# Performance work log

Hardware: AMD Instinct MI355X
Metric: run time of the kernel (lower is better)

Reference implementation:

```python
import jax, jax.numpy as jnp
import numpy as np

EPS = 1e-6
H = 12  # num_heads


def _rms(x, w):
    return x / jnp.sqrt(jnp.mean(x * x, axis=-1, keepdims=True) + EPS) * w


def _rot_half(x):
    x1, x2 = jnp.split(x, 2, axis=-1)
    return jnp.concatenate([-x2, x1], axis=-1)


def _rope(t, cos, sin):
    # t: [B,H,N,hd]; cos/sin: [N,hd] broadcast
    return t * cos + _rot_half(t) * sin


def setup_inputs() -> dict:
    key = jax.random.key(0)
    B, N, D, Nc = 1, 2048, 768, 16
    hd = D // H
    mh = 4 * D
    ks = jax.random.split(key, 16)
    s = 0.02
    g = lambda k, shape, sc=1.0: jax.random.normal(k, shape, dtype=jnp.float32) * sc
    # real RoPE tables (half-duplicated layout to match rotate_half)
    inv = 1.0 / (10000.0 ** (np.arange(hd // 2, dtype=np.float64) / (hd // 2)))
    ang = np.arange(N, dtype=np.float64)[:, None] * inv[None, :]
    cos = jnp.asarray(np.concatenate([np.cos(ang), np.cos(ang)], -1), dtype=jnp.float32)
    sin = jnp.asarray(np.concatenate([np.sin(ang), np.sin(ang)], -1), dtype=jnp.float32)
    return {
        'x': g(ks[0], (B, N, D)),
        'c': g(ks[1], (B, D)),
        'cond': g(ks[2], (B, Nc, D)),
        'rope_cos': cos,
        'rope_sin': sin,
        'norm1_w': jnp.ones((D,), jnp.float32),
        'norm2_w': jnp.ones((D,), jnp.float32),
        'norm3_w': jnp.ones((D,), jnp.float32),
        'cond_norm_w': jnp.ones((D,), jnp.float32),
        'sa_qkv_w': g(ks[3], (3 * D, D), s),
        'sa_proj_w': g(ks[4], (D, D), s),
        'sa_proj_b': jnp.zeros((D,), jnp.float32),
        'sa_qn_w': jnp.ones((hd,), jnp.float32),
        'sa_kn_w': jnp.ones((hd,), jnp.float32),
        'ca_q_w': g(ks[5], (D, D), s),
        'ca_k_w': g(ks[6], (D, D), s),
        'ca_v_w': g(ks[7], (D, D), s),
        'ca_proj_w': g(ks[8], (D, D), s),
        'ca_proj_b': jnp.zeros((D,), jnp.float32),
        'ca_qn_w': jnp.ones((hd,), jnp.float32),
        'ca_kn_w': jnp.ones((hd,), jnp.float32),
        'mlp_w1': g(ks[9], (mh, D), s),
        'mlp_w2': g(ks[10], (D, mh), s),
        'mlp_w3': g(ks[11], (mh, D), s),
        'ada_w': g(ks[12], (9 * D, D), s),
        'ada_b': jnp.zeros((9 * D,), jnp.float32),
    }


def reference(x, c, cond, rope_cos, rope_sin, norm1_w, norm2_w, norm3_w, cond_norm_w,
              sa_qkv_w, sa_proj_w, sa_proj_b, sa_qn_w, sa_kn_w,
              ca_q_w, ca_k_w, ca_v_w, ca_proj_w, ca_proj_b, ca_qn_w, ca_kn_w,
              mlp_w1, mlp_w2, mlp_w3, ada_w, ada_b):
    B, N, D = x.shape
    hd = D // H
    scale = hd ** -0.5

    # adaLN modulation: SiLU(c) -> Linear -> 9 chunks of [B, D]
    mod = jax.nn.silu(c) @ ada_w.T + ada_b
    (sh_msa, sc_msa, g_msa, sh_ca, sc_ca, g_ca,
     sh_mlp, sc_mlp, g_mlp) = jnp.split(mod, 9, axis=1)

    def modulate(h, sh, sc):
        return h * (1.0 + sc[:, None, :]) + sh[:, None, :]

    # ---- self-attention with QK-norm + RoPE ----
    h = modulate(_rms(x, norm1_w), sh_msa, sc_msa)
    qkv = (h @ sa_qkv_w.T).reshape(B, N, 3, H, hd).transpose(2, 0, 3, 1, 4)  # [3,B,H,N,hd]
    q, k, v = qkv[0], qkv[1], qkv[2]
    q = _rope(_rms(q, sa_qn_w), rope_cos, rope_sin)
    k = _rope(_rms(k, sa_kn_w), rope_cos, rope_sin)
    attn = jax.nn.softmax(jnp.einsum('bhid,bhjd->bhij', q, k) * scale, axis=-1)
    o = jnp.einsum('bhij,bhjd->bhid', attn, v).transpose(0, 2, 1, 3).reshape(B, N, D)
    x = x + g_msa[:, None, :] * (o @ sa_proj_w.T + sa_proj_b)

    # ---- cross-attention (RoPE on q only) ----
    h = modulate(_rms(x, norm2_w), sh_ca, sc_ca)
    cn = _rms(cond, cond_norm_w)
    Nc = cond.shape[1]
    q = (h @ ca_q_w.T).reshape(B, N, H, hd).transpose(0, 2, 1, 3)
    k = (cn @ ca_k_w.T).reshape(B, Nc, H, hd).transpose(0, 2, 1, 3)
    v = (cn @ ca_v_w.T).reshape(B, Nc, H, hd).transpose(0, 2, 1, 3)
    q = _rope(_rms(q, ca_qn_w), rope_cos, rope_sin)
    k = _rms(k, ca_kn_w)
    attn = jax.nn.softmax(jnp.einsum('bhid,bhjd->bhij', q, k) * scale, axis=-1)
    o = jnp.einsum('bhij,bhjd->bhid', attn, v).transpose(0, 2, 1, 3).reshape(B, N, D)
    x = x + g_ca[:, None, :] * (o @ ca_proj_w.T + ca_proj_b)

    # ---- SwiGLU MLP ----
    h = modulate(_rms(x, norm3_w), sh_mlp, sc_mlp)
    x = x + g_mlp[:, None, :] * ((jax.nn.silu(h @ mlp_w1.T) * (h @ mlp_w3.T)) @ mlp_w2.T)
    return x
```

## Files before the change

### kernel.cpp

```cpp
#include <hip/hip_runtime.h>

typedef unsigned short u16;
typedef unsigned int u32;
typedef __attribute__((ext_vector_type(8))) short s16x8;
typedef __attribute__((ext_vector_type(4))) float f32x4;
typedef __attribute__((ext_vector_type(4))) int i32x4;

#define PS 1572864

#define OFF_SAQKV  0
#define OFF_SAPROJ 1769472
#define OFF_CAQ    2359296
#define OFF_CAPROJ 2949120
#define OFF_W1     3538944
#define OFF_W2     5898240
#define OFF_W3     8257536

static __device__ __forceinline__ float bf2f(u16 u) {
    return __uint_as_float(((u32)u) << 16);
}
static __device__ __forceinline__ u16 f2bf(float f) {
    u32 x = __float_as_uint(f);
    return (u16)((x + 0x7fffu + ((x >> 16) & 1u)) >> 16);
}
static __device__ __forceinline__ i32x4 pack8(float4 a, float4 b) {
    u32 p0 = (u32)f2bf(a.x) | ((u32)f2bf(a.y) << 16);
    u32 p1 = (u32)f2bf(a.z) | ((u32)f2bf(a.w) << 16);
    u32 p2 = (u32)f2bf(b.x) | ((u32)f2bf(b.y) << 16);
    u32 p3 = (u32)f2bf(b.z) | ((u32)f2bf(b.w) << 16);
    return (i32x4){(int)p0, (int)p1, (int)p2, (int)p3};
}
static __device__ __forceinline__ float wave_sum(float v) {
#pragma unroll
    for (int off = 32; off > 0; off >>= 1) v += __shfl_xor(v, off);
    return v;
}
static __device__ __forceinline__ void gload16(const void* g, void* l) {
    __builtin_amdgcn_global_load_lds((const __attribute__((address_space(1))) void*)g,
                                     (__attribute__((address_space(3))) void*)l, 16, 0, 0);
}

__global__ __launch_bounds__(256) void cvt_ada(const float* __restrict__ s0,
                                               const float* __restrict__ s1,
                                               const float* __restrict__ s2,
                                               const float* __restrict__ s3,
                                               const float* __restrict__ s4,
                                               const float* __restrict__ s5,
                                               const float* __restrict__ s6,
                                               u16* __restrict__ wall,
                                               const float* __restrict__ c,
                                               const float* __restrict__ adaw,
                                               const float* __restrict__ adab,
                                               float* __restrict__ mod) {
    const int bid = blockIdx.x;
    const int tid = threadIdx.x;
    if (bid < 5184) {
        int u = bid * 256 + tid;
        const float* src;
        int rel;
        if (u < 221184)       { src = s0; rel = u; }
        else if (u < 294912)  { src = s1; rel = u - 221184; }
        else if (u < 368640)  { src = s2; rel = u - 294912; }
        else if (u < 442368)  { src = s3; rel = u - 368640; }
        else if (u < 737280)  { src = s4; rel = u - 442368; }
        else if (u < 1032192) { src = s5; rel = u - 737280; }
        else                  { src = s6; rel = u - 1032192; }
        float4 a = *(const float4*)(src + (size_t)rel * 8);
        float4 b = *(const float4*)(src + (size_t)rel * 8 + 4);
        *(i32x4*)(wall + (size_t)u * 8) = pack8(a, b);
    } else {
        int wid = (bid - 5184) * 4 + (tid >> 6);
        int lane = tid & 63;
        float sum = 0.f;
#pragma unroll
        for (int i = 0; i < 12; ++i) {
            float cv = c[i * 64 + lane];
            cv = cv / (1.f + __expf(-cv));
            sum += cv * adaw[(size_t)wid * 768 + i * 64 + lane];
        }
        sum = wave_sum(sum);
        if (lane == 0) mod[wid] = sum + adab[wid];
    }
}

__global__ __launch_bounds__(256) void rms_mod(const float* __restrict__ x,
                                               const float* __restrict__ w,
                                               const float* __restrict__ mod, int chunk,
                                               u16* __restrict__ out) {
    const int row = blockIdx.x;
    const int tid = threadIdx.x;
    const float* xr = x + (size_t)row * 768;
    float v0 = xr[tid], v1 = xr[256 + tid], v2 = xr[512 + tid];
    float ss = wave_sum(v0 * v0 + v1 * v1 + v2 * v2);
    __shared__ float red[4];
    if ((tid & 63) == 0) red[tid >> 6] = ss;
    __syncthreads();
    float rn = rsqrtf((red[0] + red[1] + red[2] + red[3]) * (1.f / 768.f) + 1e-6f);
    const float* sh = mod + chunk * 768;
    const float* sc = sh + 768;
    u16* orow = out + (size_t)row * 768;
    orow[tid]       = f2bf(v0 * rn * w[tid]       * (1.f + sc[tid])       + sh[tid]);
    orow[256 + tid] = f2bf(v1 * rn * w[256 + tid] * (1.f + sc[256 + tid]) + sh[256 + tid]);
    orow[512 + tid] = f2bf(v2 * rn * w[512 + tid] * (1.f + sc[512 + tid]) + sh[512 + tid]);
}

template <int EPI, int BN>
__global__ __launch_bounds__(256) void gemm_bt4(const u16* __restrict__ A,
                                                const u16* __restrict__ Wb,
                                                int M, int N, int K,
                                                float* outf, u16* outb,
                                                const float* resid,
                                                const float* __restrict__ gate,
                                                const float* __restrict__ bias,
                                                int C, int R, int nxc) {
    constexpr int NB = BN / 32;
    __shared__ __align__(16) u16 As[2][128 * 32];
    __shared__ __align__(16) u16 Bs[2][BN * 32];
    const int tid = threadIdx.x;
    const int lane = tid & 63;
    const int w = tid >> 6;
    const int wr = w >> 1, wc = w & 1;
    const int sub = blockIdx.x;
    const int xcd = sub & 7, idx = sub >> 3;
    const int cx = xcd % nxc, cy = xcd / nxc;
    const int col0 = (cx * C + idx % C) * BN;
    const int row0 = (cy * R + idx / C) << 7;

    const int r0u = tid >> 2, s0u = (tid & 3) ^ (r0u & 3);
    const int r1u = (tid + 256) >> 2, s1u = (tid & 3) ^ (r1u & 3);
    const u16* a0 = A + (size_t)(row0 + r0u) * K + s0u * 8;
    const u16* a1 = A + (size_t)(row0 + r1u) * K + s1u * 8;
    const u16* b0 = Wb + (size_t)(col0 + r0u) * K + s0u * 8;
    const u16* b1 = Wb + (size_t)(col0 + r1u) * K + s1u * 8;

    f32x4 acc[4][NB];
#pragma unroll
    for (int m = 0; m < 4; ++m)
#pragma unroll
        for (int n = 0; n < NB; ++n) acc[m][n] = (f32x4){0.f, 0.f, 0.f, 0.f};

    const int nt = K >> 5;
    int cur = 0;
#define G4_STAGE(buf, k0)                                   \
    {                                                       \
        char* ad = (char*)As[buf] + w * 1024;               \
        char* bd = (char*)Bs[buf] + w * 1024;               \
        gload16(a0 + (k0), ad);                             \
        gload16(a1 + (k0), ad + 4096);                      \
        gload16(b0 + (k0), bd);                             \
        if constexpr (BN == 128) gload16(b1 + (k0), bd + 4096); \
    }
    G4_STAGE(0, 0)
    for (int t = 0; t < nt; ++t) {
        __syncthreads();
        if (t + 1 < nt) G4_STAGE(cur ^ 1, (t + 1) << 5)
        s16x8 af[4], bfv[NB];
#pragma unroll
        for (int m = 0; m < 4; ++m) {
            int ra = wr * 64 + m * 16 + (lane & 15);
            int u = (lane >> 4) ^ (ra & 3);
            af[m] = *(const s16x8*)((const char*)As[cur] + ra * 64 + u * 16);
        }
#pragma unroll
        for (int n = 0; n < NB; ++n) {
            int cb = wc * (BN / 2) + n * 16 + (lane & 15);
            int u = (lane >> 4) ^ (cb & 3);
            bfv[n] = *(const s16x8*)((const char*)Bs[cur] + cb * 64 + u * 16);
        }
#pragma unroll
        for (int m = 0; m < 4; ++m)
#pragma unroll
            for (int n = 0; n < NB; ++n)
                acc[m][n] = __builtin_amdgcn_mfma_f32_16x16x32_bf16(af[m], bfv[n], acc[m][n], 0, 0, 0);
        cur ^= 1;
    }
#undef G4_STAGE
#pragma unroll
    for (int m = 0; m < 4; ++m) {
#pragma unroll
        for (int n = 0; n < NB; ++n) {
#pragma unroll
            for (int i = 0; i < 4; ++i) {
                int r = row0 + wr * 64 + m * 16 + (lane >> 4) * 4 + i;
                int cc = col0 + wc * (BN / 2) + n * 16 + (lane & 15);
                size_t idx2 = (size_t)r * N + cc;
                float v = acc[m][n][i];
                if constexpr (EPI == 0) {
                    outf[idx2] = v;
                } else if constexpr (EPI == 1) {
                    outb[idx2] = f2bf(v);
                } else if constexpr (EPI == 2) {
                    float b = bias ? bias[cc] : 0.f;
                    outf[idx2] = resid[idx2] + gate[cc] * (v + b);
                }
            }
        }
    }
}

__global__ __launch_bounds__(256) void gemm_sk4(const u16* __restrict__ A,
                                                const u16* __restrict__ Wb,
                                                int M, int N, int K,
                                                u16* __restrict__ pz,
                                                int C, int R, int nxc,
                                                int nsub, int kslice) {
    __shared__ __align__(16) u16 As[2][128 * 32];
    __shared__ __align__(16) u16 Bs[2][64 * 32];
    const int tid = threadIdx.x;
    const int lane = tid & 63;
    const int w = tid >> 6;
    const int wr = w >> 1, wc = w & 1;
    const int sub = blockIdx.x % nsub;
    const int z = blockIdx.x / nsub;
    const int xcd = sub & 7, idx = sub >> 3;
    const int cx = xcd % nxc, cy = xcd / nxc;
    const int col0 = (cx * C + idx % C) << 6;
    const int row0 = (cy * R + idx / C) << 7;
    const int kbase = z * kslice;

    const int r0u = tid >> 2, s0u = (tid & 3) ^ (r0u & 3);
    const int r1u = (tid + 256) >> 2, s1u = (tid & 3) ^ (r1u & 3);
    const u16* a0 = A + (size_t)(row0 + r0u) * K + kbase + s0u * 8;
    const u16* a1 = A + (size_t)(row0 + r1u) * K + kbase + s1u * 8;
    const u16* b0 = Wb + (size_t)(col0 + r0u) * K + kbase + s0u * 8;

    f32x4 acc[4][2];
#pragma unroll
    for (int m = 0; m < 4; ++m)
#pragma unroll
        for (int n = 0; n < 2; ++n) acc[m][n] = (f32x4){0.f, 0.f, 0.f, 0.f};

    const int nt = kslice >> 5;
    int cur = 0;
#define SK_STAGE(buf, k0)                                   \
    {                                                       \
        char* ad = (char*)As[buf] + w * 1024;               \
        char* bd = (char*)Bs[buf] + w * 1024;               \
        gload16(a0 + (k0), ad);                             \
        gload16(a1 + (k0), ad + 4096);                      \
        gload16(b0 + (k0), bd);                             \
    }
    SK_STAGE(0, 0)
    for (int t = 0; t < nt; ++t) {
        __syncthreads();
        if (t + 1 < nt) SK_STAGE(cur ^ 1, (t + 1) << 5)
        s16x8 af[4], bfv[2];
#pragma unroll
        for (int m = 0; m < 4; ++m) {
            int ra = wr * 64 + m * 16 + (lane & 15);
            int u = (lane >> 4) ^ (ra & 3);
            af[m] = *(const s16x8*)((const char*)As[cur] + ra * 64 + u * 16);
        }
#pragma unroll
        for (int n = 0; n < 2; ++n) {
            int cb = wc * 32 + n * 16 + (lane & 15);
            int u = (lane >> 4) ^ (cb & 3);
            bfv[n] = *(const s16x8*)((const char*)Bs[cur] + cb * 64 + u * 16);
        }
#pragma unroll
        for (int m = 0; m < 4; ++m)
#pragma unroll
            for (int n = 0; n < 2; ++n)
                acc[m][n] = __builtin_amdgcn_mfma_f32_16x16x32_bf16(af[m], bfv[n], acc[m][n], 0, 0, 0);
        cur ^= 1;
    }
#undef SK_STAGE
    u16* po = pz + (size_t)z * PS;
#pragma unroll
    for (int m = 0; m < 4; ++m)
#pragma unroll
        for (int n = 0; n < 2; ++n)
#pragma unroll
            for (int i = 0; i < 4; ++i) {
                int r = row0 + wr * 64 + m * 16 + (lane >> 4) * 4 + i;
                int cc = col0 + wc * 32 + n * 16 + (lane & 15);
                po[(size_t)r * N + cc] = f2bf(acc[m][n][i]);
            }
}

template <int MODE>
__global__ __launch_bounds__(256) void comb4(const u16* __restrict__ pz,
                                             const float* __restrict__ resid,
                                             const float* __restrict__ gate,
                                             const float* __restrict__ bias,
                                             float* __restrict__ outf) {
    int base = (blockIdx.x * 256 + threadIdx.x) * 8;
    int col = base % 768;
    s16x8 p0 = *(const s16x8*)(pz + base);
    s16x8 p1 = *(const s16x8*)(pz + PS + base);
    s16x8 p2 = *(const s16x8*)(pz + 2 * PS + base);
    s16x8 p3 = *(const s16x8*)(pz + 3 * PS + base);
    float o[8];
#pragma unroll
    for (int e = 0; e < 8; ++e) {
        float s = (bf2f((u16)p0[e]) + bf2f((u16)p1[e])) +
                  (bf2f((u16)p2[e]) + bf2f((u16)p3[e]));
        if constexpr (MODE == 0) {
            o[e] = s;
        } else {
            float bb = bias ? bias[col + e] : 0.f;
            o[e] = resid[base + e] + gate[col + e] * (s + bb);
        }
    }
    *(float4*)(outf + base) = (float4){o[0], o[1], o[2], o[3]};
    *(float4*)(outf + base + 4) = (float4){o[4], o[5], o[6], o[7]};
}

__global__ __launch_bounds__(256) void comb_rms(const u16* __restrict__ pz,
                                                const float* __restrict__ resid,
                                                const float* __restrict__ gate,
                                                const float* __restrict__ bias,
                                                const float* __restrict__ mod, int chunk,
                                                const float* __restrict__ w,
                                                float* __restrict__ outf,
                                                u16* __restrict__ outb) {
    const int row = blockIdx.x;
    const int tid = threadIdx.x;
    float val[3];
    float ss = 0.f;
#pragma unroll
    for (int j = 0; j < 3; ++j) {
        int col = tid + j * 256;
        size_t ix = (size_t)row * 768 + col;
        float s = (bf2f(pz[ix]) + bf2f(pz[PS + ix])) +
                  (bf2f(pz[2 * PS + ix]) + bf2f(pz[3 * PS + ix]));
        float bb = bias ? bias[col] : 0.f;
        float v = resid[ix] + gate[col] * (s + bb);
        val[j] = v;
        ss += v * v;
        outf[ix] = v;
    }
    ss = wave_sum(ss);
    __shared__ float red[4];
    if ((tid & 63) == 0) red[tid >> 6] = ss;
    __syncthreads();
    float rn = rsqrtf((red[0] + red[1] + red[2] + red[3]) * (1.f / 768.f) + 1e-6f);
    const float* sh = mod + chunk * 768;
    const float* sc = sh + 768;
#pragma unroll
    for (int j = 0; j < 3; ++j) {
        int col = tid + j * 256;
        size_t ix = (size_t)row * 768 + col;
        outb[ix] = f2bf(val[j] * rn * w[col] * (1.f + sc[col]) + sh[col]);
    }
}

__global__ __launch_bounds__(256) void comb_qrope(const u16* __restrict__ pz,
                                                  const float* __restrict__ qnw,
                                                  const float* __restrict__ cosT,
                                                  const float* __restrict__ sinT,
                                                  float* __restrict__ qb) {
    int wid = blockIdx.x * 4 + (threadIdx.x >> 6);
    int lane = threadIdx.x & 63;
    int n = wid / 12, h = wid % 12;
    size_t ix = (size_t)n * 768 + h * 64 + lane;
    float v = (bf2f(pz[ix]) + bf2f(pz[PS + ix])) +
              (bf2f(pz[2 * PS + ix]) + bf2f(pz[3 * PS + ix]));
    float ss = wave_sum(v * v);
    float vn = v * rsqrtf(ss * (1.f / 64.f) + 1e-6f) * qnw[lane];
    float part = __shfl_xor(vn, 32);
    float rot = (lane < 32) ? -part : part;
    qb[ix] = vn * cosT[n * 64 + lane] + rot * sinT[n * 64 + lane];
}

__global__ __launch_bounds__(256) void gemm_w13(const u16* __restrict__ A,
                                                const u16* __restrict__ W1,
                                                const u16* __restrict__ W3,
                                                int M, int N, int K,
                                                u16* __restrict__ outb,
                                                int C, int R, int nxc) {
    __shared__ __align__(16) u16 As[2][128 * 32];
    __shared__ __align__(16) u16 B1s[2][64 * 32];
    __shared__ __align__(16) u16 B3s[2][64 * 32];
    const int tid = threadIdx.x;
    const int lane = tid & 63;
    const int w = tid >> 6;
    const int wr = w >> 1, wc = w & 1;
    const int sub = blockIdx.x;
    const int xcd = sub & 7, idx = sub >> 3;
    const int cx = xcd % nxc, cy = xcd / nxc;
    const int col0 = (cx * C + idx % C) << 6;
    const int row0 = (cy * R + idx / C) << 7;

    const int r0u = tid >> 2, s0u = (tid & 3) ^ (r0u & 3);
    const int r1u = (tid + 256) >> 2, s1u = (tid & 3) ^ (r1u & 3);
    const u16* a0 = A + (size_t)(row0 + r0u) * K + s0u * 8;
    const u16* a1 = A + (size_t)(row0 + r1u) * K + s1u * 8;
    const u16* b1p = W1 + (size_t)(col0 + r0u) * K + s0u * 8;
    const u16* b3p = W3 + (size_t)(col0 + r0u) * K + s0u * 8;

    f32x4 acc1[4][2], acc3[4][2];
#pragma unroll
    for (int m = 0; m < 4; ++m)
#pragma unroll
        for (int n = 0; n < 2; ++n) {
            acc1[m][n] = (f32x4){0.f, 0.f, 0.f, 0.f};
            acc3[m][n] = (f32x4){0.f, 0.f, 0.f, 0.f};
        }

    const int nt = K >> 5;
    int cur = 0;
#define W13_STAGE(buf, k0)                                  \
    {                                                       \
        char* ad = (char*)As[buf] + w * 1024;               \
        char* bd1 = (char*)B1s[buf] + w * 1024;             \
        char* bd3 = (char*)B3s[buf] + w * 1024;             \
        gload16(a0 + (k0), ad);                             \
        gload16(a1 + (k0), ad + 4096);                      \
        gload16(b1p + (k0), bd1);                           \
        gload16(b3p + (k0), bd3);                           \
    }
    W13_STAGE(0, 0)
    for (int t = 0; t < nt; ++t) {
        __syncthreads();
        if (t + 1 < nt) W13_STAGE(cur ^ 1, (t + 1) << 5)
        s16x8 af[4], b1v[2], b3v[2];
#pragma unroll
        for (int m = 0; m < 4; ++m) {
            int ra = wr * 64 + m * 16 + (lane & 15);
            int u = (lane >> 4) ^ (ra & 3);
            af[m] = *(const s16x8*)((const char*)As[cur] + ra * 64 + u * 16);
        }
#pragma unroll
        for (int n = 0; n < 2; ++n) {
            int cb = wc * 32 + n * 16 + (lane & 15);
            int u = (lane >> 4) ^ (cb & 3);
            b1v[n] = *(const s16x8*)((const char*)B1s[cur] + cb * 64 + u * 16);
            b3v[n] = *(const s16x8*)((const char*)B3s[cur] + cb * 64 + u * 16);
        }
#pragma unroll
        for (int m = 0; m < 4; ++m)
#pragma unroll
            for (int n = 0; n < 2; ++n) {
                acc1[m][n] = __builtin_amdgcn_mfma_f32_16x16x32_bf16(af[m], b1v[n], acc1[m][n], 0, 0, 0);
                acc3[m][n] = __builtin_amdgcn_mfma_f32_16x16x32_bf16(af[m], b3v[n], acc3[m][n], 0, 0, 0);
            }
        cur ^= 1;
    }
#undef W13_STAGE
#pragma unroll
    for (int m = 0; m < 4; ++m)
#pragma unroll
        for (int n = 0; n < 2; ++n)
#pragma unroll
            for (int i = 0; i < 4; ++i) {
                int r = row0 + wr * 64 + m * 16 + (lane >> 4) * 4 + i;
                int cc = col0 + wc * 32 + n * 16 + (lane & 15);
                float v1 = acc1[m][n][i];
                float g = v1 / (1.f + __expf(-v1));
                outb[(size_t)r * N + cc] = f2bf(g * acc3[m][n][i]);
            }
}

__global__ __launch_bounds__(256) void qk_prep(u16* __restrict__ qkv,
                                               u16* __restrict__ vT,
                                               const float* __restrict__ qnw,
                                               const float* __restrict__ knw,
                                               const float* __restrict__ cosT,
                                               const float* __restrict__ sinT) {
    const int bid = blockIdx.x;
    const int tid = threadIdx.x;
    if (bid < 12288) {
        int wid = bid * 4 + (tid >> 6);
        int lane = tid & 63;
        int n = wid / 24;
        int rem = wid % 24;
        int which = rem / 12;
        int h = rem % 12;
        u16* p = qkv + (size_t)n * 2304 + which * 768 + h * 64 + lane;
        float v = bf2f(*p);
        float ss = wave_sum(v * v);
        const float* wv = which ? knw : qnw;
        float vn = v * rsqrtf(ss * (1.f / 64.f) + 1e-6f) * wv[lane];
        float part = __shfl_xor(vn, 32);
        float rot = (lane < 32) ? -part : part;
        *p = f2bf(vn * cosT[n * 64 + lane] + rot * sinT[n * 64 + lane]);
    } else {
        const int b2 = bid - 12288;
        const int kt = b2 & 31, h = b2 >> 5;
        __shared__ __align__(16) u16 tt[64][72];
        {
            int key = tid >> 2, qq = tid & 3;
            const u16* src = qkv + (size_t)(kt * 64 + key) * 2304 + 1536 + h * 64 + qq * 16;
            *(i32x4*)&tt[key][qq * 16]     = *(const i32x4*)src;
            *(i32x4*)&tt[key][qq * 16 + 8] = *(const i32x4*)(src + 8);
        }
        __syncthreads();
        {
            int d = tid >> 2, kq = tid & 3;
            s16x8 o0, o1;
#pragma unroll
            for (int e = 0; e < 8; ++e) o0[e] = (short)tt[kq * 16 + e][d];
#pragma unroll
            for (int e = 0; e < 8; ++e) o1[e] = (short)tt[kq * 16 + 8 + e][d];
            u16* dst = vT + (size_t)h * 131072 + (size_t)d * 2048 + kt * 64 + kq * 16;
            *(s16x8*)dst = o0;
            *(s16x8*)(dst + 8) = o1;
        }
    }
}

__global__ __launch_bounds__(256) void sa_attn_mfma(const u16* __restrict__ qkv,
                                                    const u16* __restrict__ vT,
                                                    u16* __restrict__ at,
                                                    float* __restrict__ pl) {
    const int h = blockIdx.y;
    const int r0 = blockIdx.x * 64;
    const int z = blockIdx.z;
    const int tid = threadIdx.x;
    const int lane = tid & 63;
    const int w = tid >> 6;
    __shared__ __align__(16) u16 Ks[2][64 * 64];
    __shared__ __align__(16) u16 Vs[2][64 * 64];
    __shared__ __align__(16) u16 Ps[4][16 * 64];

    s16x8 qf[2];
    {
        const u16* qrow = qkv + (size_t)(r0 + w * 16 + (lane & 15)) * 2304 + h * 64 + ((lane >> 4) * 8);
        qf[0] = *(const s16x8*)qrow;
        qf[1] = *(const s16x8*)(qrow + 32);
    }
    f32x4 oacc[4];
#pragma unroll
    for (int n = 0; n < 4; ++n) oacc[n] = (f32x4){0.f, 0.f, 0.f, 0.f};
    float lp[4] = {0.f, 0.f, 0.f, 0.f};

    const u16* ksrc[2];
    const u16* vsrc[2];
#pragma unroll
    for (int j = 0; j < 2; ++j) {
        int u = (w * 2 + j) * 64 + lane;
        int row = u >> 3, seg = (u & 7) ^ (row & 7);
        ksrc[j] = qkv + (size_t)(z * 512 + row) * 2304 + 768 + h * 64 + seg * 8;
        vsrc[j] = vT + (size_t)h * 131072 + (size_t)row * 2048 + z * 512 + seg * 8;
    }

#define SA_STAGE(buf, t_)                                          \
    {                                                              \
        char* kd = (char*)Ks[buf] + w * 2048;                      \
        char* vd = (char*)Vs[buf] + w * 2048;                      \
        gload16(ksrc[0] + (size_t)(t_) * 147456, kd);              \
        gload16(ksrc[1] + (size_t)(t_) * 147456, kd + 1024);       \
        gload16(vsrc[0] + (t_) * 64, vd);                          \
        gload16(vsrc[1] + (t_) * 64, vd + 1024);                   \
    }

    SA_STAGE(0, 0)
    int cur = 0;
    for (int t = 0; t < 8; ++t) {
        __syncthreads();
        if (t + 1 < 8) SA_STAGE(cur ^ 1, t + 1)

        f32x4 sacc[4];
#pragma unroll
        for (int n = 0; n < 4; ++n) sacc[n] = (f32x4){0.f, 0.f, 0.f, 0.f};
#pragma unroll
        for (int kk = 0; kk < 2; ++kk) {
#pragma unroll
            for (int n = 0; n < 4; ++n) {
                int key = n * 16 + (lane & 15);
                int d = kk * 32 + (lane >> 4) * 8;
                int boff = key * 128 + ((d * 2) ^ ((key & 7) << 4));
                s16x8 kf = *(const s16x8*)((const char*)Ks[cur] + boff);
                sacc[n] = __builtin_amdgcn_mfma_f32_16x16x32_bf16(qf[kk], kf, sacc[n], 0, 0, 0);
            }
        }
#pragma unroll
        for (int n = 0; n < 4; ++n) {
#pragma unroll
            for (int i = 0; i < 4; ++i) {
                float p = __expf(fmaf(sacc[n][i], 0.125f, -8.0f));
                lp[i] += p;
                int row = (lane >> 4) * 4 + i;
                int key = n * 16 + (lane & 15);
                int boff = row * 128 + ((key * 2) ^ ((row & 7) << 4));
                *(u16*)((char*)Ps[w] + boff) = f2bf(p);
            }
        }
#pragma unroll
        for (int kk = 0; kk < 2; ++kk) {
            int koff = kk * 32 + (lane >> 4) * 8;
            int prow = lane & 15;
            int pboff = prow * 128 + ((koff * 2) ^ ((prow & 7) << 4));
            s16x8 pf = *(const s16x8*)((const char*)Ps[w] + pboff);
#pragma unroll
            for (int n = 0; n < 4; ++n) {
                int d = n * 16 + (lane & 15);
                int vboff = d * 128 + ((koff * 2) ^ ((d & 7) << 4));
                s16x8 vf = *(const s16x8*)((const char*)Vs[cur] + vboff);
                oacc[n] = __builtin_amdgcn_mfma_f32_16x16x32_bf16(pf, vf, oacc[n], 0, 0, 0);
            }
        }
        cur ^= 1;
    }
#undef SA_STAGE
#pragma unroll
    for (int off = 1; off < 16; off <<= 1) {
#pragma unroll
        for (int i = 0; i < 4; ++i) lp[i] += __shfl_xor(lp[i], off);
    }
    u16* po = at + (size_t)z * PS;
#pragma unroll
    for (int n = 0; n < 4; ++n) {
#pragma unroll
        for (int i = 0; i < 4; ++i) {
            int r = r0 + w * 16 + (lane >> 4) * 4 + i;
            int d = n * 16 + (lane & 15);
            po[(size_t)r * 768 + h * 64 + d] = f2bf(oacc[n][i]);
        }
    }
    if ((lane & 15) == 0) {
#pragma unroll
        for (int i = 0; i < 4; ++i) {
            int r = r0 + w * 16 + (lane >> 4) * 4 + i;
            pl[z * 24576 + h * 2048 + r] = lp[i];
        }
    }
}

__global__ __launch_bounds__(256) void sa_combine4(const u16* __restrict__ at,
                                                   const float* __restrict__ pl,
                                                   u16* __restrict__ obuf) {
    int idx = blockIdx.x * 256 + threadIdx.x;
    int base = idx * 8;
    int row = base / 768;
    int col = base % 768;
    int h = col >> 6;
    float l = (pl[h * 2048 + row] + pl[24576 + h * 2048 + row]) +
              (pl[49152 + h * 2048 + row] + pl[73728 + h * 2048 + row]);
    float inv = 1.f / l;
    s16x8 a = *(const s16x8*)(at + base);
    s16x8 b = *(const s16x8*)(at + PS + base);
    s16x8 cc = *(const s16x8*)(at + 2 * PS + base);
    s16x8 d = *(const s16x8*)(at + 3 * PS + base);
    s16x8 o;
#pragma unroll
    for (int e = 0; e < 8; ++e) {
        float s = (bf2f((u16)a[e]) + bf2f((u16)b[e])) +
                  (bf2f((u16)cc[e]) + bf2f((u16)d[e]));
        o[e] = (short)f2bf(s * inv);
    }
    *(s16x8*)(obuf + base) = o;
}

__global__ __launch_bounds__(256) void ca_attn(const float* __restrict__ qb,
                                               const float* __restrict__ kca,
                                               const float* __restrict__ vca,
                                               u16* __restrict__ obuf) {
    int wid = blockIdx.x * 4 + (threadIdx.x >> 6);
    int lane = threadIdx.x & 63;
    int n = wid / 12, h = wid % 12;
    float qd = qb[(size_t)n * 768 + h * 64 + lane] * 0.125f;
    float s[16];
#pragma unroll
    for (int j = 0; j < 16; ++j) {
        float part = qd * kca[(size_t)j * 768 + h * 64 + lane];
        s[j] = wave_sum(part);
    }
    float mm = s[0];
#pragma unroll
    for (int j = 1; j < 16; ++j) mm = fmaxf(mm, s[j]);
    float l = 0.f;
#pragma unroll
    for (int j = 0; j < 16; ++j) { s[j] = __expf(s[j] - mm); l += s[j]; }
    float od = 0.f;
#pragma unroll
    for (int j = 0; j < 16; ++j) od += s[j] * vca[(size_t)j * 768 + h * 64 + lane];
    obuf[(size_t)n * 768 + h * 64 + lane] = f2bf(od / l);
}

__global__ __launch_bounds__(256) void cak_rms(float* __restrict__ kca,
                                               const float* __restrict__ knw) {
    int wid = blockIdx.x * 4 + (threadIdx.x >> 6);
    int lane = threadIdx.x & 63;
    int n = wid / 12, h = wid % 12;
    float* p = kca + (size_t)n * 768 + h * 64 + lane;
    float v = *p;
    float ss = wave_sum(v * v);
    *p = v * rsqrtf(ss * (1.f / 64.f) + 1e-6f) * knw[lane];
}

__global__ __launch_bounds__(256) void small_gemm_f(const float* __restrict__ cond,
                                                    const float* __restrict__ cnw,
                                                    const float* __restrict__ cakw,
                                                    const float* __restrict__ cavw,
                                                    float* __restrict__ kca,
                                                    float* __restrict__ vca) {
    int wid = blockIdx.x * 4 + (threadIdx.x >> 6);
    int lane = threadIdx.x & 63;
    int which = wid / 12288;
    int rem = wid % 12288;
    int rrow = rem / 768;
    int ocol = rem % 768;
    float cv[12];
    float ss = 0.f;
#pragma unroll
    for (int i = 0; i < 12; ++i) {
        cv[i] = cond[(size_t)rrow * 768 + i * 64 + lane];
        ss += cv[i] * cv[i];
    }
    ss = wave_sum(ss);
    float rn = rsqrtf(ss * (1.f / 768.f) + 1e-6f);
    const float* Wm = which ? cavw : cakw;
    float sum = 0.f;
#pragma unroll
    for (int i = 0; i < 12; ++i)
        sum += cv[i] * rn * cnw[i * 64 + lane] * Wm[(size_t)ocol * 768 + i * 64 + lane];
    sum = wave_sum(sum);
    if (lane == 0) (which ? vca : kca)[(size_t)rrow * 768 + ocol] = sum;
}

extern "C" void kernel_launch(void* const* d_in, const int* in_sizes, int n_in,
                              void* d_out, int out_size, void* d_ws, size_t ws_size,
                              hipStream_t stream) {
    const float* x     = (const float*)d_in[0];
    const float* c     = (const float*)d_in[1];
    const float* cond  = (const float*)d_in[2];
    const float* cosT  = (const float*)d_in[3];
    const float* sinT  = (const float*)d_in[4];
    const float* n1w   = (const float*)d_in[5];
    const float* n2w   = (const float*)d_in[6];
    const float* n3w   = (const float*)d_in[7];
    const float* cnw   = (const float*)d_in[8];
    const float* saqkvw  = (const float*)d_in[9];
    const float* saprojw = (const float*)d_in[10];
    const float* saprojb = (const float*)d_in[11];
    const float* saqnw   = (const float*)d_in[12];
    const float* saknw   = (const float*)d_in[13];
    const float* caqw    = (const float*)d_in[14];
    const float* cakw    = (const float*)d_in[15];
    const float* cavw    = (const float*)d_in[16];
    const float* caprojw = (const float*)d_in[17];
    const float* caprojb = (const float*)d_in[18];
    const float* caqnw   = (const float*)d_in[19];
    const float* caknw   = (const float*)d_in[20];
    const float* w1      = (const float*)d_in[21];
    const float* w2      = (const float*)d_in[22];
    const float* w3      = (const float*)d_in[23];
    const float* adaw    = (const float*)d_in[24];
    const float* adab    = (const float*)d_in[25];
    float* out = (float*)d_out;
    char* ws = (char*)d_ws;

    float* mod  = (float*)ws;
    u16* hbuf   = (u16*)(ws + 32768);
    u16* obuf   = (u16*)(ws + 3178496);
    char* R1    = ws + 6324224;
    u16* qkvb   = (u16*)R1;
    u16* vTb    = (u16*)(R1 + 9437184);
    float* qbuf = (float*)R1;
    u16* gbuf   = (u16*)R1;
    float* kca  = (float*)(ws + 18956288);
    float* vca  = (float*)(ws + 19005440);
    u16* WALL   = (u16*)(ws + 19054592);
    u16* AT     = (u16*)(ws + 40288256);
    float* PL4  = (float*)(ws + 52871168);
    u16* SKP    = (u16*)(ws + 53264384);

    cvt_ada<<<6912, 256, 0, stream>>>(saqkvw, saprojw, caqw, caprojw, w1, w2, w3,
                                      WALL, c, adaw, adab, mod);

    rms_mod<<<2048, 256, 0, stream>>>(x, n1w, mod, 0, hbuf);
    gemm_bt4<1, 64><<<576, 256, 0, stream>>>(hbuf, WALL + OFF_SAQKV, 2048, 2304, 768,
                                             nullptr, qkvb, nullptr, nullptr, nullptr,
                                             9, 8, 4);
    qk_prep<<<12672, 256, 0, stream>>>(qkvb, vTb, saqnw, saknw, cosT, sinT);
    sa_attn_mfma<<<dim3(32, 12, 4), 256, 0, stream>>>(qkvb, vTb, AT, PL4);
    sa_combine4<<<768, 256, 0, stream>>>(AT, PL4, obuf);
    gemm_sk4<<<768, 256, 0, stream>>>(obuf, WALL + OFF_SAPROJ, 2048, 768, 768,
                                      SKP, 6, 4, 2, 192, 192);
    comb_rms<<<2048, 256, 0, stream>>>(SKP, x, mod + 2 * 768, saprojb,
                                       mod, 3, n2w, out, hbuf);

    gemm_sk4<<<768, 256, 0, stream>>>(hbuf, WALL + OFF_CAQ, 2048, 768, 768,
                                      SKP, 6, 4, 2, 192, 192);
    comb_qrope<<<6144, 256, 0, stream>>>(SKP, caqnw, cosT, sinT, qbuf);
    small_gemm_f<<<6144, 256, 0, stream>>>(cond, cnw, cakw, cavw, kca, vca);
    cak_rms<<<48, 256, 0, stream>>>(kca, caknw);
    ca_attn<<<6144, 256, 0, stream>>>(qbuf, kca, vca, obuf);
    gemm_sk4<<<768, 256, 0, stream>>>(obuf, WALL + OFF_CAPROJ, 2048, 768, 768,
                                      SKP, 6, 4, 2, 192, 192);
    comb_rms<<<2048, 256, 0, stream>>>(SKP, out, mod + 5 * 768, caprojb,
                                       mod, 6, n3w, out, hbuf);

    gemm_w13<<<768, 256, 0, stream>>>(hbuf, WALL + OFF_W1, WALL + OFF_W3,
                                      2048, 3072, 768, gbuf, 12, 8, 4);
    gemm_sk4<<<768, 256, 0, stream>>>(gbuf, WALL + OFF_W2, 2048, 768, 3072,
                                      SKP, 6, 4, 2, 192, 768);
    comb4<2><<<768, 256, 0, stream>>>(SKP, out, mod + 8 * 768, nullptr, out);
}
```

Baseline: 222.3 us.

## Fuse QK norm, RoPE and V transpose into QKV GEMM epilogue; fold cond K/V into prologue

The QKV GEMM epilogue now stages each 128x64 tile in shared memory. There it applies per-head RMS norm and RoPE to the Q and K columns, and writes a transposed V copy directly, so the separate qk_prep kernel and its extra pass over qkv are gone. The cross-attention K/V projection of cond, together with its K RMS norm, moves into extra blocks of the initial conversion kernel, removing two launches. In exchange the GEMM epilogue carries more shared-memory traffic and a serial per-thread loop over 32 elements.

```diff
diff --git a/kernel.cpp b/kernel.cpp
--- a/kernel.cpp
+++ b/kernel.cpp
@@ -51,7 +51,14 @@
                                                const float* __restrict__ c,
                                                const float* __restrict__ adaw,
                                                const float* __restrict__ adab,
-                                               float* __restrict__ mod) {
+                                               float* __restrict__ mod,
+                                               const float* __restrict__ cond,
+                                               const float* __restrict__ cnw,
+                                               const float* __restrict__ cakw,
+                                               const float* __restrict__ cavw,
+                                               const float* __restrict__ caknw,
+                                               float* __restrict__ kca,
+                                               float* __restrict__ vca) {
     const int bid = blockIdx.x;
     const int tid = threadIdx.x;
     if (bid < 5184) {
@@ -68,7 +75,7 @@
         float4 a = *(const float4*)(src + (size_t)rel * 8);
         float4 b = *(const float4*)(src + (size_t)rel * 8 + 4);
         *(i32x4*)(wall + (size_t)u * 8) = pack8(a, b);
-    } else {
+    } else if (bid < 6912) {
         int wid = (bid - 5184) * 4 + (tid >> 6);
         int lane = tid & 63;
         float sum = 0.f;
@@ -80,6 +87,46 @@
         }
         sum = wave_sum(sum);
         if (lane == 0) mod[wid] = sum + adab[wid];
+    } else {
+        int b = bid - 6912;
+        int which = b / 192;
+        int rem = b % 192;
+        int rrow = rem / 12, h = rem % 12;
+        int w = tid >> 6, lane = tid & 63;
+        __shared__ float kvsh[64];
+        float cv[12];
+        float ss = 0.f;
+#pragma unroll
+        for (int i = 0; i < 12; ++i) {
+            cv[i] = cond[(size_t)rrow * 768 + i * 64 + lane];
+            ss += cv[i] * cv[i];
+        }
+        ss = wave_sum(ss);
+        float rn = rsqrtf(ss * (1.f / 768.f) + 1e-6f);
+#pragma unroll
+        for (int i = 0; i < 12; ++i) cv[i] = cv[i] * rn * cnw[i * 64 + lane];
+        const float* Wm = which ? cavw : cakw;
+#pragma unroll
+        for (int j = 0; j < 16; ++j) {
+            int ocol = h * 64 + w * 16 + j;
+            float d = 0.f;
+#pragma unroll
+            for (int i = 0; i < 12; ++i)
+                d += cv[i] * Wm[(size_t)ocol * 768 + i * 64 + lane];
+            d = wave_sum(d);
+            if (lane == 0) kvsh[w * 16 + j] = d;
+        }
+        __syncthreads();
+        if (tid < 64) {
+            float v = kvsh[lane];
+            if (which == 0) {
+                float sk = wave_sum(v * v);
+                v = v * rsqrtf(sk * (1.f / 64.f) + 1e-6f) * caknw[lane];
+                kca[(size_t)rrow * 768 + h * 64 + lane] = v;
+            } else {
+                vca[(size_t)rrow * 768 + h * 64 + lane] = v;
+            }
+        }
     }
 }
 
@@ -104,18 +151,19 @@
     orow[512 + tid] = f2bf(v2 * rn * w[512 + tid] * (1.f + sc[512 + tid]) + sh[512 + tid]);
 }
 
-template <int EPI, int BN>
-__global__ __launch_bounds__(256) void gemm_bt4(const u16* __restrict__ A,
+__global__ __launch_bounds__(256) void gemm_qkv(const u16* __restrict__ A,
                                                 const u16* __restrict__ Wb,
-                                                int M, int N, int K,
-                                                float* outf, u16* outb,
-                                                const float* resid,
-                                                const float* __restrict__ gate,
-                                                const float* __restrict__ bias,
+                                                u16* __restrict__ qkvb,
+                                                u16* __restrict__ vT,
+                                                const float* __restrict__ qnw,
+                                                const float* __restrict__ knw,
+                                                const float* __restrict__ cosT,
+                                                const float* __restrict__ sinT,
                                                 int C, int R, int nxc) {
-    constexpr int NB = BN / 32;
-    __shared__ __align__(16) u16 As[2][128 * 32];
-    __shared__ __align__(16) u16 Bs[2][BN * 32];
+    constexpr int K = 768, N = 2304;
+    __shared__ __align__(16) char smem[33792];
+    u16 (*As)[128 * 32] = (u16(*)[128 * 32])smem;
+    u16 (*Bs)[64 * 32] = (u16(*)[64 * 32])(smem + 16384);
     const int tid = threadIdx.x;
     const int lane = tid & 63;
     const int w = tid >> 6;
@@ -123,7 +171,7 @@
     const int sub = blockIdx.x;
     const int xcd = sub & 7, idx = sub >> 3;
     const int cx = xcd % nxc, cy = xcd / nxc;
-    const int col0 = (cx * C + idx % C) * BN;
+    const int col0 = (cx * C + idx % C) << 6;
     const int row0 = (cy * R + idx / C) << 7;
 
     const int r0u = tid >> 2, s0u = (tid & 3) ^ (r0u & 3);
@@ -131,30 +179,28 @@
     const u16* a0 = A + (size_t)(row0 + r0u) * K + s0u * 8;
     const u16* a1 = A + (size_t)(row0 + r1u) * K + s1u * 8;
     const u16* b0 = Wb + (size_t)(col0 + r0u) * K + s0u * 8;
-    const u16* b1 = Wb + (size_t)(col0 + r1u) * K + s1u * 8;
-
-    f32x4 acc[4][NB];
+
+    f32x4 acc[4][2];
 #pragma unroll
     for (int m = 0; m < 4; ++m)
 #pragma unroll
-        for (int n = 0; n < NB; ++n) acc[m][n] = (f32x4){0.f, 0.f, 0.f, 0.f};
+        for (int n = 0; n < 2; ++n) acc[m][n] = (f32x4){0.f, 0.f, 0.f, 0.f};
 
     const int nt = K >> 5;
     int cur = 0;
-#define G4_STAGE(buf, k0)                                   \
+#define QKV_STAGE(buf, k0)                                  \
     {                                                       \
         char* ad = (char*)As[buf] + w * 1024;               \
         char* bd = (char*)Bs[buf] + w * 1024;               \
         gload16(a0 + (k0), ad);                             \
         gload16(a1 + (k0), ad + 4096);                      \
         gload16(b0 + (k0), bd);                             \
-        if constexpr (BN == 128) gload16(b1 + (k0), bd + 4096); \
-    }
-    G4_STAGE(0, 0)
+    }
+    QKV_STAGE(0, 0)
     for (int t = 0; t < nt; ++t) {
         __syncthreads();
-        if (t + 1 < nt) G4_STAGE(cur ^ 1, (t + 1) << 5)
-        s16x8 af[4], bfv[NB];
+        if (t + 1 < nt) QKV_STAGE(cur ^ 1, (t + 1) << 5)
+        s16x8 af[4], bfv[2];
 #pragma unroll
         for (int m = 0; m < 4; ++m) {
             int ra = wr * 64 + m * 16 + (lane & 15);
@@ -162,38 +208,78 @@
             af[m] = *(const s16x8*)((const char*)As[cur] + ra * 64 + u * 16);
         }
 #pragma unroll
-        for (int n = 0; n < NB; ++n) {
-            int cb = wc * (BN / 2) + n * 16 + (lane & 15);
+        for (int n = 0; n < 2; ++n) {
+            int cb = wc * 32 + n * 16 + (lane & 15);
             int u = (lane >> 4) ^ (cb & 3);
             bfv[n] = *(const s16x8*)((const char*)Bs[cur] + cb * 64 + u * 16);
         }
 #pragma unroll
         for (int m = 0; m < 4; ++m)
 #pragma unroll
-            for (int n = 0; n < NB; ++n)
+            for (int n = 0; n < 2; ++n)
                 acc[m][n] = __builtin_amdgcn_mfma_f32_16x16x32_bf16(af[m], bfv[n], acc[m][n], 0, 0, 0);
         cur ^= 1;
     }
-#undef G4_STAGE
-#pragma unroll
-    for (int m = 0; m < 4; ++m) {
-#pragma unroll
-        for (int n = 0; n < NB; ++n) {
-#pragma unroll
-            for (int i = 0; i < 4; ++i) {
-                int r = row0 + wr * 64 + m * 16 + (lane >> 4) * 4 + i;
-                int cc = col0 + wc * (BN / 2) + n * 16 + (lane & 15);
-                size_t idx2 = (size_t)r * N + cc;
-                float v = acc[m][n][i];
-                if constexpr (EPI == 0) {
-                    outf[idx2] = v;
-                } else if constexpr (EPI == 1) {
-                    outb[idx2] = f2bf(v);
-                } else if constexpr (EPI == 2) {
-                    float b = bias ? bias[cc] : 0.f;
-                    outf[idx2] = resid[idx2] + gate[cc] * (v + b);
+#undef QKV_STAGE
+    __syncthreads();
+
+    const int region = col0 / 768;
+    const int h = (col0 % 768) >> 6;
+    if (region < 2) {
+        float (*T)[66] = (float(*)[66])smem;
+#pragma unroll
+        for (int m = 0; m < 4; ++m)
+#pragma unroll
+            for (int n = 0; n < 2; ++n)
+#pragma unroll
+                for (int i = 0; i < 4; ++i)
+                    T[wr * 64 + m * 16 + (lane >> 4) * 4 + i]
+                     [wc * 32 + n * 16 + (lane & 15)] = acc[m][n][i];
+        __syncthreads();
+        const float* wv = region ? knw : qnw;
+        const int rl = tid >> 1, half = (tid & 1) * 32;
+        float ss = 0.f;
+#pragma unroll
+        for (int d = 0; d < 32; ++d) {
+            float v = T[rl][half + d];
+            ss += v * v;
+        }
+        ss += __shfl_xor(ss, 1);
+        float rn = rsqrtf(ss * (1.f / 64.f) + 1e-6f);
+        const int ng = row0 + rl;
+        u16* orow = qkvb + (size_t)ng * N + col0;
+        const float* cr = cosT + ng * 64;
+        const float* sr = sinT + ng * 64;
+#pragma unroll
+        for (int d = 0; d < 32; ++d) {
+            int dd = half + d;
+            float vn = T[rl][dd] * rn * wv[dd];
+            float pt = T[rl][dd ^ 32] * rn * wv[dd ^ 32];
+            float rot = (dd < 32) ? -pt : pt;
+            orow[dd] = f2bf(vn * cr[dd] + rot * sr[dd]);
+        }
+    } else {
+        u16 (*Tb)[66] = (u16(*)[66])smem;
+#pragma unroll
+        for (int m = 0; m < 4; ++m)
+#pragma unroll
+            for (int n = 0; n < 2; ++n)
+#pragma unroll
+                for (int i = 0; i < 4; ++i) {
+                    int rl = wr * 64 + m * 16 + (lane >> 4) * 4 + i;
+                    int dd = wc * 32 + n * 16 + (lane & 15);
+                    u16 b = f2bf(acc[m][n][i]);
+                    qkvb[(size_t)(row0 + rl) * N + col0 + dd] = b;
+                    Tb[rl][dd] = b;
                 }
-            }
+        __syncthreads();
+        u16* dst = vT + (size_t)h * 131072 + (size_t)lane * 2048 + row0 + w * 32;
+#pragma unroll
+        for (int g = 0; g < 4; ++g) {
+            s16x8 o;
+#pragma unroll
+            for (int e = 0; e < 8; ++e) o[e] = (short)Tb[w * 32 + g * 8 + e][lane];
+            *(s16x8*)(dst + g * 8) = o;
         }
     }
 }
@@ -452,54 +538,6 @@
             }
 }
 
-__global__ __launch_bounds__(256) void qk_prep(u16* __restrict__ qkv,
-                                               u16* __restrict__ vT,
-                                               const float* __restrict__ qnw,
-                                               const float* __restrict__ knw,
-                                               const float* __restrict__ cosT,
-                                               const float* __restrict__ sinT) {
-    const int bid = blockIdx.x;
-    const int tid = threadIdx.x;
-    if (bid < 12288) {
-        int wid = bid * 4 + (tid >> 6);
-        int lane = tid & 63;
-        int n = wid / 24;
-        int rem = wid % 24;
-        int which = rem / 12;
-        int h = rem % 12;
-        u16* p = qkv + (size_t)n * 2304 + which * 768 + h * 64 + lane;
-        float v = bf2f(*p);
-        float ss = wave_sum(v * v);
-        const float* wv = which ? knw : qnw;
-        float vn = v * rsqrtf(ss * (1.f / 64.f) + 1e-6f) * wv[lane];
-        float part = __shfl_xor(vn, 32);
-        float rot = (lane < 32) ? -part : part;
-        *p = f2bf(vn * cosT[n * 64 + lane] + rot * sinT[n * 64 + lane]);
-    } else {
-        const int b2 = bid - 12288;
-        const int kt = b2 & 31, h = b2 >> 5;
-        __shared__ __align__(16) u16 tt[64][72];
-        {
-            int key = tid >> 2, qq = tid & 3;
-            const u16* src = qkv + (size_t)(kt * 64 + key) * 2304 + 1536 + h * 64 + qq * 16;
-            *(i32x4*)&tt[key][qq * 16]     = *(const i32x4*)src;
-            *(i32x4*)&tt[key][qq * 16 + 8] = *(const i32x4*)(src + 8);
-        }
-        __syncthreads();
-        {
-            int d = tid >> 2, kq = tid & 3;
-            s16x8 o0, o1;
-#pragma unroll
-            for (int e = 0; e < 8; ++e) o0[e] = (short)tt[kq * 16 + e][d];
-#pragma unroll
-            for (int e = 0; e < 8; ++e) o1[e] = (short)tt[kq * 16 + 8 + e][d];
-            u16* dst = vT + (size_t)h * 131072 + (size_t)d * 2048 + kt * 64 + kq * 16;
-            *(s16x8*)dst = o0;
-            *(s16x8*)(dst + 8) = o1;
-        }
-    }
-}
-
 __global__ __launch_bounds__(256) void sa_attn_mfma(const u16* __restrict__ qkv,
                                                     const u16* __restrict__ vT,
                                                     u16* __restrict__ at,
@@ -667,47 +705,6 @@
 #pragma unroll
     for (int j = 0; j < 16; ++j) od += s[j] * vca[(size_t)j * 768 + h * 64 + lane];
     obuf[(size_t)n * 768 + h * 64 + lane] = f2bf(od / l);
-}
-
-__global__ __launch_bounds__(256) void cak_rms(float* __restrict__ kca,
-                                               const float* __restrict__ knw) {
-    int wid = blockIdx.x * 4 + (threadIdx.x >> 6);
-    int lane = threadIdx.x & 63;
-    int n = wid / 12, h = wid % 12;
-    float* p = kca + (size_t)n * 768 + h * 64 + lane;
-    float v = *p;
-    float ss = wave_sum(v * v);
-    *p = v * rsqrtf(ss * (1.f / 64.f) + 1e-6f) * knw[lane];
-}
-
-__global__ __launch_bounds__(256) void small_gemm_f(const float* __restrict__ cond,
-                                                    const float* __restrict__ cnw,
-                                                    const float* __restrict__ cakw,
-                                                    const float* __restrict__ cavw,
-                                                    float* __restrict__ kca,
-                                                    float* __restrict__ vca) {
-    int wid = blockIdx.x * 4 + (threadIdx.x >> 6);
-    int lane = threadIdx.x & 63;
-    int which = wid / 12288;
-    int rem = wid % 12288;
-    int rrow = rem / 768;
-    int ocol = rem % 768;
-    float cv[12];
-    float ss = 0.f;
-#pragma unroll
-    for (int i = 0; i < 12; ++i) {
-        cv[i] = cond[(size_t)rrow * 768 + i * 64 + lane];
-        ss += cv[i] * cv[i];
-    }
-    ss = wave_sum(ss);
-    float rn = rsqrtf(ss * (1.f / 768.f) + 1e-6f);
-    const float* Wm = which ? cavw : cakw;
-    float sum = 0.f;
-#pragma unroll
-    for (int i = 0; i < 12; ++i)
-        sum += cv[i] * rn * cnw[i * 64 + lane] * Wm[(size_t)ocol * 768 + i * 64 + lane];
-    sum = wave_sum(sum);
-    if (lane == 0) (which ? vca : kca)[(size_t)rrow * 768 + ocol] = sum;
 }
 
 extern "C" void kernel_launch(void* const* d_in, const int* in_sizes, int n_in,
@@ -757,14 +754,13 @@
     float* PL4  = (float*)(ws + 52871168);
     u16* SKP    = (u16*)(ws + 53264384);
 
-    cvt_ada<<<6912, 256, 0, stream>>>(saqkvw, saprojw, caqw, caprojw, w1, w2, w3,
-                                      WALL, c, adaw, adab, mod);
+    cvt_ada<<<7296, 256, 0, stream>>>(saqkvw, saprojw, caqw, caprojw, w1, w2, w3,
+                                      WALL, c, adaw, adab, mod,
+                                      cond, cnw, cakw, cavw, caknw, kca, vca);
 
     rms_mod<<<2048, 256, 0, stream>>>(x, n1w, mod, 0, hbuf);
-    gemm_bt4<1, 64><<<576, 256, 0, stream>>>(hbuf, WALL + OFF_SAQKV, 2048, 2304, 768,
-                                             nullptr, qkvb, nullptr, nullptr, nullptr,
-                                             9, 8, 4);
-    qk_prep<<<12672, 256, 0, stream>>>(qkvb, vTb, saqnw, saknw, cosT, sinT);
+    gemm_qkv<<<576, 256, 0, stream>>>(hbuf, WALL + OFF_SAQKV, qkvb, vTb,
+                                      saqnw, saknw, cosT, sinT, 9, 8, 4);
     sa_attn_mfma<<<dim3(32, 12, 4), 256, 0, stream>>>(qkvb, vTb, AT, PL4);
     sa_combine4<<<768, 256, 0, stream>>>(AT, PL4, obuf);
     gemm_sk4<<<768, 256, 0, stream>>>(obuf, WALL + OFF_SAPROJ, 2048, 768, 768,
@@ -775,8 +771,6 @@
     gemm_sk4<<<768, 256, 0, stream>>>(hbuf, WALL + OFF_CAQ, 2048, 768, 768,
                                       SKP, 6, 4, 2, 192, 192);
     comb_qrope<<<6144, 256, 0, stream>>>(SKP, caqnw, cosT, sinT, qbuf);
-    small_gemm_f<<<6144, 256, 0, stream>>>(cond, cnw, cakw, cavw, kca, vca);
-    cak_rms<<<48, 256, 0, stream>>>(kca, caknw);
     ca_attn<<<6144, 256, 0, stream>>>(qbuf, kca, vca, obuf);
     gemm_sk4<<<768, 256, 0, stream>>>(obuf, WALL + OFF_CAPROJ, 2048, 768, 768,
                                       SKP, 6, 4, 2, 192, 192);
```

Result: no change. 220.8 us (-0.7%).
